# Kernel tuning notes

Measured on AMD Instinct MI355X. Metric: run time of the kernel, lower is better.

Reference implementation:

```python
import jax, jax.numpy as jnp
import numpy as np

B, C, H, W = 16384, 1, 2048, 1
HID = 5


def setup_inputs() -> dict:
    key = jax.random.key(0)
    kx, kl, k1, k2, k3, k4 = jax.random.split(key, 6)
    x = jax.random.normal(kx, (B, C, H, W), dtype=jnp.float32)
    # random ragged lengths in [1, H]; zero out padded tail so the module's
    # (x != 0).any(dim=2) mask recovers exactly these lengths
    lengths = jax.random.randint(kl, (B,), 1, H + 1)
    t_idx = jnp.arange(H)
    valid = (t_idx[None, :] < lengths[:, None])  # [B, H]
    x = x * valid[:, None, :, None].astype(jnp.float32)
    s = 1.0 / np.sqrt(HID)
    W_ih = jax.random.uniform(k1, (4 * HID, 1), minval=-s, maxval=s, dtype=jnp.float32)
    W_hh = jax.random.uniform(k2, (4 * HID, HID), minval=-s, maxval=s, dtype=jnp.float32)
    b_ih = jax.random.uniform(k3, (4 * HID,), minval=-s, maxval=s, dtype=jnp.float32)
    b_hh = jax.random.uniform(k4, (4 * HID,), minval=-s, maxval=s, dtype=jnp.float32)
    return {"x": x, "W_ih": W_ih, "W_hh": W_hh, "b_ih": b_ih, "b_hh": b_hh}


def reference(x, W_ih, W_hh, b_ih, b_hh):
    b, c, h, w = x.shape
    feats = c * w  # == 1 (LSTM input_size)
    xr = x.reshape(b, h, feats)  # [B, T, 1]
    mask = jnp.any(xr != 0, axis=2)  # [B, T]
    lengths = mask.sum(axis=1).astype(jnp.int32)  # [B]

    bias = b_ih + b_hh  # [4H]
    # precompute input projection for all timesteps: [B, T, 4H]
    x_proj = jnp.einsum('btf,gf->btg', xr, W_ih) + bias
    xs = jnp.moveaxis(x_proj, 1, 0)  # [T, B, 4H]

    h0 = jnp.zeros((b, HID), dtype=x.dtype)
    c0 = jnp.zeros((b, HID), dtype=x.dtype)

    def step(carry, inp):
        hp, cp = carry
        xg, t = inp
        gates = xg + hp @ W_hh.T  # [B, 4H]
        i, f, g, o = jnp.split(gates, 4, axis=1)
        i = jax.nn.sigmoid(i)
        f = jax.nn.sigmoid(f)
        g = jnp.tanh(g)
        o = jax.nn.sigmoid(o)
        cn = f * cp + i * g
        hn = o * jnp.tanh(cn)
        # packed semantics: only advance state while t < length (per sample)
        upd = (t < lengths)[:, None]
        hn = jnp.where(upd, hn, hp)
        cn = jnp.where(upd, cn, cp)
        return (hn, cn), None

    (hT, cT), _ = jax.lax.scan(step, (h0, c0), (xs, jnp.arange(h)))
    return hT[None]  # [1, B, HID] matching torch h shape
```

## Files before the change

kernel.cpp:

```cpp
#include <hip/hip_runtime.h>

#define Bn   16384
#define Tn   2048
#define HIDn 5

static __device__ __forceinline__ float rcp_fast(float v) {
    return __builtin_amdgcn_rcpf(v);
}
static __device__ __forceinline__ float exp2_fast(float v) {
    return __builtin_amdgcn_exp2f(v);
}

template <int K>
static __device__ __forceinline__ float bcast8(float v) {
    return __int_as_float(
        __builtin_amdgcn_ds_swizzle(__float_as_int(v), (K << 5) | 0x18));
}

__global__ __launch_bounds__(256) void len_kernel(const float* __restrict__ x,
                                                  int* __restrict__ lengths) {
    const int gtid = blockIdx.x * 256 + threadIdx.x;
    const int row  = gtid >> 6;
    const int lane = threadIdx.x & 63;
    const float4* r = reinterpret_cast<const float4*>(x + (size_t)row * Tn);
    int cnt = 0;
    #pragma unroll
    for (int i = 0; i < Tn / 4 / 64; ++i) {
        float4 v = r[i * 64 + lane];
        cnt += (v.x != 0.0f) + (v.y != 0.0f) + (v.z != 0.0f) + (v.w != 0.0f);
    }
    #pragma unroll
    for (int off = 32; off > 0; off >>= 1) cnt += __shfl_xor(cnt, off, 64);
    if (lane == 0) lengths[row] = cnt;
}

__global__ __launch_bounds__(256, 2) void lstm_kernel(const float* __restrict__ x,
                                                      const float* __restrict__ Wih,
                                                      const float* __restrict__ Whh,
                                                      const float* __restrict__ bih,
                                                      const float* __restrict__ bhh,
                                                      const int* __restrict__ lengths,
                                                      float* __restrict__ out) {
    const int gtid = blockIdx.x * 256 + threadIdx.x;
    const int b    = gtid >> 3;
    const int lsub = threadIdx.x & 7;
    const int k    = min(lsub, 4);

    const float L2E   = 1.4426950408889634f;
    const float NL2E2 = -2.0f * L2E;

    float wih[4], bias[4], whh[4][HIDn];
    #pragma unroll
    for (int j = 0; j < 4; ++j) {
        const int   gi = 5 * j + k;
        const float sj = (j == 2) ? NL2E2 : -L2E;
        wih[j]  = Wih[gi] * sj;
        bias[j] = (bih[gi] + bhh[gi]) * sj;
        #pragma unroll
        for (int kk = 0; kk < HIDn; ++kk) whh[j][kk] = Whh[gi * HIDn + kk] * sj;
    }

    const int len = lengths[b];
    const float* xrow = x + (size_t)b * Tn;

    float h0 = 0, h1 = 0, h2 = 0, h3 = 0, h4 = 0;
    float h_own = 0, c = 0;

    float4 xq = *reinterpret_cast<const float4*>(xrow);
    int t = 0;
    while (__any(t < len)) {
        const float4 xn = *reinterpret_cast<const float4*>(xrow + min(t + 4, Tn - 4));
        const float xs[4] = { xq.x, xq.y, xq.z, xq.w };

        #pragma unroll
        for (int s = 0; s < 4; ++s) {
            if (t + s < len) {
                const float xv = xs[s];

                float p[4];
                #pragma unroll
                for (int j = 0; j < 4; ++j) {
                    float pp = fmaf(xv, wih[j], bias[j]);
                    pp = fmaf(h0, whh[j][0], pp);
                    pp = fmaf(h1, whh[j][1], pp);
                    pp = fmaf(h2, whh[j][2], pp);
                    pp = fmaf(h3, whh[j][3], pp);
                    pp = fmaf(h4, whh[j][4], pp);
                    p[j] = pp;
                }
                const float e0 = exp2_fast(p[0]);
                const float e1 = exp2_fast(p[1]);
                const float e2 = exp2_fast(p[2]);
                const float e3 = exp2_fast(p[3]);
                const float x0 = 1.0f + e0, x1 = 1.0f + e1;
                const float x2 = 1.0f + e2, x3 = 1.0f + e3;
                const float r01 = rcp_fast(x0 * x1);
                const float r23 = rcp_fast(x2 * x3);
                const float gi_ = x1 * r01;
                const float gf_ = x0 * r01;
                const float gg_ = fmaf(2.0f, x3 * r23, -1.0f);
                const float go_ = x2 * r23;

                c = fmaf(gf_, c, gi_ * gg_);

                const float ec = exp2_fast(c * NL2E2);
                const float th = fmaf(2.0f, rcp_fast(1.0f + ec), -1.0f);
                h_own = go_ * th;

                h0 = bcast8<0>(h_own);
                h1 = bcast8<1>(h_own);
                h2 = bcast8<2>(h_own);
                h3 = bcast8<3>(h_own);
                h4 = bcast8<4>(h_own);
            }
        }
        xq = xn;
        t += 4;
    }

    if (lsub < HIDn) out[b * HIDn + lsub] = h_own;
}

extern "C" void kernel_launch(void* const* d_in, const int* in_sizes, int n_in,
                              void* d_out, int out_size, void* d_ws, size_t ws_size,
                              hipStream_t stream) {
    const float* x   = (const float*)d_in[0];
    const float* Wih = (const float*)d_in[1];
    const float* Whh = (const float*)d_in[2];
    const float* bih = (const float*)d_in[3];
    const float* bhh = (const float*)d_in[4];
    float* out = (float*)d_out;
    int* lengths = (int*)d_ws;

    len_kernel<<<Bn / 4, 256, 0, stream>>>(x, lengths);
    lstm_kernel<<<Bn * 8 / 256, 256, 0, stream>>>(x, Wih, Whh, bih, bhh, lengths, out);
}
```

Baseline: 610.8 us.

## Sort sequences by length and schedule them dynamically per 8-lane group

Adds a single-block counting sort that orders sequences by descending length. The LSTM kernel now has each 8-lane group pull its next sequence from a global atomic counter, and the group writes its result before taking more work. The aim is to cut wavefront divergence from mixed lengths and to balance the load across groups. In exchange it adds an extra serial kernel launch, atomics, and control-flow overhead inside the recurrent loop.

```diff
diff --git a/kernel.cpp b/kernel.cpp
--- a/kernel.cpp
+++ b/kernel.cpp
@@ -1,8 +1,9 @@
 #include <hip/hip_runtime.h>
 
-#define Bn   16384
-#define Tn   2048
-#define HIDn 5
+#define Bn    16384
+#define Tn    2048
+#define HIDn  5
+#define NBINS 2048
 
 static __device__ __forceinline__ float rcp_fast(float v) {
     return __builtin_amdgcn_rcpf(v);
@@ -15,6 +16,10 @@
 static __device__ __forceinline__ float bcast8(float v) {
     return __int_as_float(
         __builtin_amdgcn_ds_swizzle(__float_as_int(v), (K << 5) | 0x18));
+}
+template <int K>
+static __device__ __forceinline__ int bcast8i(int v) {
+    return __builtin_amdgcn_ds_swizzle(v, (K << 5) | 0x18);
 }
 
 __global__ __launch_bounds__(256) void len_kernel(const float* __restrict__ x,
@@ -34,15 +39,55 @@
     if (lane == 0) lengths[row] = cnt;
 }
 
+__global__ __launch_bounds__(1024) void sort_kernel(const int* __restrict__ lengths,
+                                                    int* __restrict__ perm,
+                                                    int* __restrict__ ctr) {
+    __shared__ int bins[NBINS];
+    __shared__ int bsum[1024];
+    const int tid = threadIdx.x;
+    bins[tid] = 0;
+    bins[tid + 1024] = 0;
+    if (tid == 0) *ctr = 0;
+    __syncthreads();
+    for (int i = tid; i < Bn; i += 1024) {
+        int d = NBINS - lengths[i];
+        d = max(0, min(NBINS - 1, d));
+        atomicAdd(&bins[d], 1);
+    }
+    __syncthreads();
+    const int a0 = bins[2 * tid], a1 = bins[2 * tid + 1];
+    const int s = a0 + a1;
+    bsum[tid] = s;
+    __syncthreads();
+    int acc = s;
+    for (int off = 1; off < 1024; off <<= 1) {
+        int v = (tid >= off) ? bsum[tid - off] : 0;
+        __syncthreads();
+        acc += v;
+        bsum[tid] = acc;
+        __syncthreads();
+    }
+    const int excl = acc - s;
+    bins[2 * tid]     = excl;
+    bins[2 * tid + 1] = excl + a0;
+    __syncthreads();
+    for (int i = tid; i < Bn; i += 1024) {
+        int d = NBINS - lengths[i];
+        d = max(0, min(NBINS - 1, d));
+        const int p = atomicAdd(&bins[d], 1);
+        perm[p] = i;
+    }
+}
+
 __global__ __launch_bounds__(256, 2) void lstm_kernel(const float* __restrict__ x,
                                                       const float* __restrict__ Wih,
                                                       const float* __restrict__ Whh,
                                                       const float* __restrict__ bih,
                                                       const float* __restrict__ bhh,
                                                       const int* __restrict__ lengths,
+                                                      const int* __restrict__ perm,
+                                                      int* __restrict__ ctr,
                                                       float* __restrict__ out) {
-    const int gtid = blockIdx.x * 256 + threadIdx.x;
-    const int b    = gtid >> 3;
     const int lsub = threadIdx.x & 7;
     const int k    = min(lsub, 4);
 
@@ -60,65 +105,76 @@
         for (int kk = 0; kk < HIDn; ++kk) whh[j][kk] = Whh[gi * HIDn + kk] * sj;
     }
 
-    const int len = lengths[b];
-    const float* xrow = x + (size_t)b * Tn;
-
+    bool dead = false, have = false;
+    int  b = 0, len = 0, t = 0;
+    const float* xrow = x;
     float h0 = 0, h1 = 0, h2 = 0, h3 = 0, h4 = 0;
     float h_own = 0, c = 0;
+    float4 xq = make_float4(0.f, 0.f, 0.f, 0.f);
 
-    float4 xq = *reinterpret_cast<const float4*>(xrow);
-    int t = 0;
-    while (__any(t < len)) {
-        const float4 xn = *reinterpret_cast<const float4*>(xrow + min(t + 4, Tn - 4));
-        const float xs[4] = { xq.x, xq.y, xq.z, xq.w };
-
-        #pragma unroll
-        for (int s = 0; s < 4; ++s) {
-            if (t + s < len) {
-                const float xv = xs[s];
-
-                float p[4];
-                #pragma unroll
-                for (int j = 0; j < 4; ++j) {
-                    float pp = fmaf(xv, wih[j], bias[j]);
-                    pp = fmaf(h0, whh[j][0], pp);
-                    pp = fmaf(h1, whh[j][1], pp);
-                    pp = fmaf(h2, whh[j][2], pp);
-                    pp = fmaf(h3, whh[j][3], pp);
-                    pp = fmaf(h4, whh[j][4], pp);
-                    p[j] = pp;
-                }
-                const float e0 = exp2_fast(p[0]);
-                const float e1 = exp2_fast(p[1]);
-                const float e2 = exp2_fast(p[2]);
-                const float e3 = exp2_fast(p[3]);
-                const float x0 = 1.0f + e0, x1 = 1.0f + e1;
-                const float x2 = 1.0f + e2, x3 = 1.0f + e3;
-                const float r01 = rcp_fast(x0 * x1);
-                const float r23 = rcp_fast(x2 * x3);
-                const float gi_ = x1 * r01;
-                const float gf_ = x0 * r01;
-                const float gg_ = fmaf(2.0f, x3 * r23, -1.0f);
-                const float go_ = x2 * r23;
-
-                c = fmaf(gf_, c, gi_ * gg_);
-
-                const float ec = exp2_fast(c * NL2E2);
-                const float th = fmaf(2.0f, rcp_fast(1.0f + ec), -1.0f);
-                h_own = go_ * th;
-
-                h0 = bcast8<0>(h_own);
-                h1 = bcast8<1>(h_own);
-                h2 = bcast8<2>(h_own);
-                h3 = bcast8<3>(h_own);
-                h4 = bcast8<4>(h_own);
+    while (__any(!dead)) {
+        if (!dead && t >= len) {
+            if (have && lsub < HIDn) out[(size_t)b * HIDn + lsub] = h_own;
+            int pos = 0;
+            if (lsub == 0) pos = atomicAdd(ctr, 1);
+            pos = bcast8i<0>(pos);
+            if (pos < Bn) {
+                b    = perm[pos];
+                len  = lengths[b];
+                xrow = x + (size_t)b * Tn;
+                t = 0; c = 0; h_own = 0;
+                h0 = h1 = h2 = h3 = h4 = 0;
+                xq = *reinterpret_cast<const float4*>(xrow);
+                have = true;
+            } else {
+                dead = true; have = false; len = 0;
             }
         }
-        xq = xn;
-        t += 4;
+        if (!dead) {
+            const float4 xn = *reinterpret_cast<const float4*>(xrow + min(t + 4, Tn - 4));
+            const float xs[4] = { xq.x, xq.y, xq.z, xq.w };
+            #pragma unroll
+            for (int s = 0; s < 4; ++s) {
+                if (t + s < len) {
+                    const float xv = xs[s];
+                    float p[4];
+                    #pragma unroll
+                    for (int j = 0; j < 4; ++j) {
+                        float pp = fmaf(xv, wih[j], bias[j]);
+                        pp = fmaf(h0, whh[j][0], pp);
+                        pp = fmaf(h1, whh[j][1], pp);
+                        pp = fmaf(h2, whh[j][2], pp);
+                        pp = fmaf(h3, whh[j][3], pp);
+                        pp = fmaf(h4, whh[j][4], pp);
+                        p[j] = pp;
+                    }
+                    const float x0 = 1.0f + exp2_fast(p[0]);
+                    const float x1 = 1.0f + exp2_fast(p[1]);
+                    const float x2 = 1.0f + exp2_fast(p[2]);
+                    const float x3 = 1.0f + exp2_fast(p[3]);
+                    const float r01 = rcp_fast(x0 * x1);
+                    const float r23 = rcp_fast(x2 * x3);
+                    const float gi_ = x1 * r01;
+                    const float gf_ = x0 * r01;
+                    const float gg_ = fmaf(2.0f, x3 * r23, -1.0f);
+                    const float go_ = x2 * r23;
+
+                    c = fmaf(gf_, c, gi_ * gg_);
+
+                    const float th = fmaf(2.0f, rcp_fast(1.0f + exp2_fast(c * NL2E2)), -1.0f);
+                    h_own = go_ * th;
+
+                    h0 = bcast8<0>(h_own);
+                    h1 = bcast8<1>(h_own);
+                    h2 = bcast8<2>(h_own);
+                    h3 = bcast8<3>(h_own);
+                    h4 = bcast8<4>(h_own);
+                }
+            }
+            xq = xn;
+            t += 4;
+        }
     }
-
-    if (lsub < HIDn) out[b * HIDn + lsub] = h_own;
 }
 
 extern "C" void kernel_launch(void* const* d_in, const int* in_sizes, int n_in,
@@ -130,8 +186,13 @@
     const float* bih = (const float*)d_in[3];
     const float* bhh = (const float*)d_in[4];
     float* out = (float*)d_out;
+
     int* lengths = (int*)d_ws;
+    int* perm    = lengths + Bn;
+    int* ctr     = perm + Bn;
 
     len_kernel<<<Bn / 4, 256, 0, stream>>>(x, lengths);
-    lstm_kernel<<<Bn * 8 / 256, 256, 0, stream>>>(x, Wih, Whh, bih, bhh, lengths, out);
+    sort_kernel<<<1, 1024, 0, stream>>>(lengths, perm, ctr);
+    lstm_kernel<<<Bn * 8 / 256, 256, 0, stream>>>(x, Wih, Whh, bih, bhh,
+                                                  lengths, perm, ctr, out);
 }
```

New measurement: 581.8 us. -4.8%, faster.
